# Optimization experiments

Measured on AMD Instinct MI355X. Metric: run time of the kernel, lower is better.

## Reference

```python
import jax, jax.numpy as jnp
import numpy as np

N_NODES = 100000
N_EDGES = 1600000
IN_F = 128
HID_F = 128
OUT_F = 128

def _glorot(key, shape):
    lim = np.sqrt(6.0 / (shape[0] + shape[1]))
    return jax.random.uniform(key, shape, jnp.float32, -lim, lim)

def setup_inputs() -> dict:
    key = jax.random.key(0)
    ks = jax.random.split(key, 9)
    x = jax.random.normal(ks[0], (N_NODES, IN_F), jnp.float32)
    src = jax.random.randint(ks[1], (N_EDGES,), 0, N_NODES, jnp.int32)
    dst = jax.random.randint(ks[2], (N_EDGES,), 0, N_NODES, jnp.int32)
    return {
        'x': x, 'src': src, 'dst': dst,
        'W_self1': _glorot(ks[3], (IN_F, HID_F)),
        'W_neigh1': _glorot(ks[4], (IN_F, HID_F)),
        'b1': jnp.zeros((HID_F,), jnp.float32),
        'W_self2': _glorot(ks[5], (HID_F, OUT_F)),
        'W_neigh2': _glorot(ks[6], (HID_F, OUT_F)),
        'b2': jnp.zeros((OUT_F,), jnp.float32),
    }

def _sage_mean(h, src, dst, W_self, W_neigh, b, n_nodes):
    # mean-aggregate src features onto dst (DGL SAGEConv 'mean')
    msg_sum = jax.ops.segment_sum(h[src], dst, num_segments=n_nodes)  # [N, d]
    deg = jax.ops.segment_sum(jnp.ones_like(dst, jnp.float32), dst, num_segments=n_nodes)
    h_neigh = msg_sum / jnp.maximum(deg, 1.0)[:, None]
    return h @ W_self + h_neigh @ W_neigh + b

def reference(x, src, dst, W_self1, W_neigh1, b1, W_self2, W_neigh2, b2):
    n = x.shape[0]
    h = _sage_mean(x, src, dst, W_self1, W_neigh1, b1, n)
    h = _sage_mean(h, src, dst, W_self2, W_neigh2, b2, n)
    # edge-wise dot product score between endpoint features (u_dot_v)
    s = jnp.sum(h[src] * h[dst], axis=-1)  # [E]
    smin, smax = jnp.min(s), jnp.max(s)
    return (s - smin) / (smax - smin)
```

## Files before the change

### kernel.cpp

```cpp
#include <hip/hip_runtime.h>
#include <hip/hip_bf16.h>

#define F 128

typedef unsigned int uint;
typedef unsigned short ushort;
typedef __attribute__((ext_vector_type(8))) short short8;
typedef __attribute__((ext_vector_type(4))) float f32x4;

__device__ inline ushort f2bf(float f) {
    uint u = __float_as_uint(f);
    u += 0x7FFF + ((u >> 16) & 1);
    return (ushort)(u >> 16);
}
__device__ inline float2 bf2f(uint u) {
    return make_float2(__uint_as_float(u << 16), __uint_as_float(u & 0xFFFF0000u));
}

__global__ __launch_bounds__(256) void rank_kernel(const int* __restrict__ dst,
                                                   int* __restrict__ cnt,
                                                   ushort* __restrict__ rel, int E) {
    int e = blockIdx.x * 256 + threadIdx.x;
    if (e < E) rel[e] = (ushort)atomicAdd(&cnt[dst[e]], 1);
}

__global__ __launch_bounds__(256) void scan_block(const int* __restrict__ cnt,
                                                  int* __restrict__ off,
                                                  int* __restrict__ bsum, int N) {
    __shared__ int t[256];
    int i = blockIdx.x * 256 + threadIdx.x;
    int v = (i < N) ? cnt[i] : 0;
    t[threadIdx.x] = v;
    __syncthreads();
    for (int o = 1; o < 256; o <<= 1) {
        int x = (threadIdx.x >= o) ? t[threadIdx.x - o] : 0;
        __syncthreads();
        t[threadIdx.x] += x;
        __syncthreads();
    }
    if (i < N) off[i] = t[threadIdx.x] - v;
    if (threadIdx.x == 255) bsum[blockIdx.x] = t[255];
}

__global__ __launch_bounds__(512) void scan_sums(int* __restrict__ bsum, int nb) {
    __shared__ int t[512];
    int v = (threadIdx.x < nb) ? bsum[threadIdx.x] : 0;
    t[threadIdx.x] = v;
    __syncthreads();
    for (int o = 1; o < 512; o <<= 1) {
        int x = (threadIdx.x >= o) ? t[threadIdx.x - o] : 0;
        __syncthreads();
        t[threadIdx.x] += x;
        __syncthreads();
    }
    if (threadIdx.x < nb) bsum[threadIdx.x] = t[threadIdx.x] - v;
}

__global__ __launch_bounds__(256) void scan_add_rdeg(int* __restrict__ off,
                                                     const int* __restrict__ bsum,
                                                     const int* __restrict__ cnt,
                                                     float* __restrict__ rdeg, int N) {
    int i = blockIdx.x * 256 + threadIdx.x;
    if (i >= N) return;
    off[i] += bsum[blockIdx.x];
    rdeg[i] = 1.0f / fmaxf((float)cnt[i], 1.0f);
}

__global__ __launch_bounds__(256) void fill_kernel(const int* __restrict__ src,
                                                   const int* __restrict__ dst,
                                                   const int* __restrict__ off,
                                                   const ushort* __restrict__ rel,
                                                   int* __restrict__ srcS, int E) {
    int e = blockIdx.x * 256 + threadIdx.x;
    if (e >= E) return;
    srcS[off[dst[e]] + (int)rel[e]] = src[e];
}

__global__ __launch_bounds__(256) void prep_kernel(const float* __restrict__ x,
                                                   const float* __restrict__ W0,
                                                   const float* __restrict__ W1,
                                                   const float* __restrict__ W2,
                                                   const float* __restrict__ W3,
                                                   uint* __restrict__ xb,
                                                   ushort* __restrict__ Wt, int NF4) {
    int i = blockIdx.x * 256 + threadIdx.x;
    if (i < NF4) {
        float4 v = ((const float4*)x)[i];
        uint ua = (uint)f2bf(v.x) | ((uint)f2bf(v.y) << 16);
        uint ub = (uint)f2bf(v.z) | ((uint)f2bf(v.w) << 16);
        ((uint2*)xb)[i] = make_uint2(ua, ub);
    } else {
        int idx = i - NF4;
        if (idx >= 4 * 16384) return;
        int j    = idx & 7;
        int lane = (idx >> 3) & 63;
        int t    = (idx >> 9) & 7;
        int kk   = (idx >> 12) & 3;
        int mat  = idx >> 14;
        int n = 16 * t + (lane & 15);
        int k = 32 * kk + 8 * (lane >> 4) + j;
        const float* W = (mat == 0) ? W0 : (mat == 1) ? W1 : (mat == 2) ? W2 : W3;
        Wt[idx] = f2bf(W[k * 128 + n]);
    }
}

__global__ __launch_bounds__(256) void agg_gather(const uint* __restrict__ hb,
                                                  const int* __restrict__ off,
                                                  const int* __restrict__ srcS,
                                                  const float* __restrict__ rdeg,
                                                  uint* __restrict__ msgb, int N, int E) {
    int node = blockIdx.x * 4 + (threadIdx.x >> 6);
    int lane = threadIdx.x & 63;
    if (node >= N) return;
    int p = off[node];
    int pe = (node == N - 1) ? E : off[node + 1];
    float2 acc = make_float2(0.f, 0.f);
    if (p < pe) {
        int deg = pe - p;
        int last = pe - 1;
        for (; p < pe; p += 8) {
            int i0 = min(p + 0, last), i1 = min(p + 1, last);
            int i2 = min(p + 2, last), i3 = min(p + 3, last);
            int i4 = min(p + 4, last), i5 = min(p + 5, last);
            int i6 = min(p + 6, last), i7 = min(p + 7, last);
            int s0 = srcS[i0], s1 = srcS[i1], s2 = srcS[i2], s3 = srcS[i3];
            int s4 = srcS[i4], s5 = srcS[i5], s6 = srcS[i6], s7 = srcS[i7];
            float2 f0 = bf2f(hb[(size_t)s0 * 64 + lane]);
            float2 f1 = bf2f(hb[(size_t)s1 * 64 + lane]);
            float2 f2 = bf2f(hb[(size_t)s2 * 64 + lane]);
            float2 f3 = bf2f(hb[(size_t)s3 * 64 + lane]);
            float2 f4 = bf2f(hb[(size_t)s4 * 64 + lane]);
            float2 f5 = bf2f(hb[(size_t)s5 * 64 + lane]);
            float2 f6 = bf2f(hb[(size_t)s6 * 64 + lane]);
            float2 f7 = bf2f(hb[(size_t)s7 * 64 + lane]);
            acc.x += ((f0.x + f1.x) + (f2.x + f3.x)) + ((f4.x + f5.x) + (f6.x + f7.x));
            acc.y += ((f0.y + f1.y) + (f2.y + f3.y)) + ((f4.y + f5.y) + (f6.y + f7.y));
        }
        int d = (8 - (deg & 7)) & 7;
        if (d) {
            float2 fl = bf2f(hb[(size_t)srcS[last] * 64 + lane]);
            float fd = (float)d;
            acc.x -= fd * fl.x;
            acc.y -= fd * fl.y;
        }
    }
    float rd = rdeg[node];
    msgb[(size_t)node * 64 + lane] = (uint)f2bf(acc.x * rd) | ((uint)f2bf(acc.y * rd) << 16);
}

__global__ __launch_bounds__(256) void sage_mfma(const uint* __restrict__ hb,
                                                 const uint* __restrict__ mb,
                                                 const uint* __restrict__ Wt,
                                                 const float* __restrict__ bias,
                                                 ushort* __restrict__ outb, int N) {
    int wave = threadIdx.x >> 6, lane = threadIdx.x & 63;
    int m = lane & 15, q = lane >> 4;
    int r0 = blockIdx.x * 64 + wave * 16;
    int arow = r0 + m;
    if (arow >= N) arow = N - 1;

    f32x4 acc[8];
#pragma unroll
    for (int t = 0; t < 8; t++) acc[t] = (f32x4){0.f, 0.f, 0.f, 0.f};

    const uint* hrow = hb + (size_t)arow * 64;
    const uint* mrow = mb + (size_t)arow * 64;
#pragma unroll
    for (int sel = 0; sel < 2; sel++) {
        const uint* arowp = sel ? mrow : hrow;
        const uint* wsel = Wt + sel * 8192;
#pragma unroll
        for (int kk = 0; kk < 4; kk++) {
            int ko = kk * 16 + q * 4;
            short8 a = *(const short8*)(arowp + ko);
#pragma unroll
            for (int t = 0; t < 8; t++) {
                short8 b = *(const short8*)(wsel + (size_t)((kk * 8 + t) * 64 + lane) * 4);
                acc[t] = __builtin_amdgcn_mfma_f32_16x16x32_bf16(a, b, acc[t], 0, 0, 0);
            }
        }
    }

#pragma unroll
    for (int t = 0; t < 8; t++) {
        float bs = bias[16 * t + m];
#pragma unroll
        for (int r = 0; r < 4; r++) {
            int orow = r0 + q * 4 + r;
            if (orow < N) outb[(size_t)orow * 128 + 16 * t + m] = f2bf(acc[t][r] + bs);
        }
    }
}

__global__ __launch_bounds__(256) void edge_score_mfma(const uint* __restrict__ hb,
                                                       const int* __restrict__ off,
                                                       const int* __restrict__ srcS,
                                                       float* __restrict__ sc,
                                                       float2* __restrict__ pmm, int N, int E) {
    int node = blockIdx.x * 4 + (threadIdx.x >> 6);
    int lane = threadIdx.x & 63;
    int m = lane & 15, q = lane >> 4;
    float lmin = INFINITY, lmax = -INFINITY;

    if (node < N) {
        int p = off[node];
        int pe = (node == N - 1) ? E : off[node + 1];
        if (p < pe) {
            const uint* nrow = hb + (size_t)node * 64;
            short8 bfr[4];
#pragma unroll
            for (int kk = 0; kk < 4; kk++)
                bfr[kk] = *(const short8*)(nrow + kk * 16 + q * 4);

            for (; p < pe; p += 16) {
                int idx = p + m;
                if (idx >= pe) idx = pe - 1;
                const uint* arow = hb + (size_t)srcS[idx] * 64;
                f32x4 acc = (f32x4){0.f, 0.f, 0.f, 0.f};
#pragma unroll
                for (int kk = 0; kk < 4; kk++) {
                    short8 a = *(const short8*)(arow + kk * 16 + q * 4);
                    acc = __builtin_amdgcn_mfma_f32_16x16x32_bf16(a, bfr[kk], acc, 0, 0, 0);
                }
                if (m == 0) {
                    if (p + 16 <= pe) {
                        *(float4*)(sc + p + q * 4) = make_float4(acc[0], acc[1], acc[2], acc[3]);
                        float mn = fminf(fminf(acc[0], acc[1]), fminf(acc[2], acc[3]));
                        float mx = fmaxf(fmaxf(acc[0], acc[1]), fmaxf(acc[2], acc[3]));
                        lmin = fminf(lmin, mn);
                        lmax = fmaxf(lmax, mx);
                    } else {
#pragma unroll
                        for (int r = 0; r < 4; r++) {
                            int e = p + q * 4 + r;
                            if (e < pe) {
                                sc[e] = acc[r];
                                lmin = fminf(lmin, acc[r]);
                                lmax = fmaxf(lmax, acc[r]);
                            }
                        }
                    }
                }
            }
        }
    }

#pragma unroll
    for (int o = 1; o <= 32; o <<= 1) {
        lmin = fminf(lmin, __shfl_xor(lmin, o));
        lmax = fmaxf(lmax, __shfl_xor(lmax, o));
    }
    __shared__ float smin[4], smax[4];
    int wv = threadIdx.x >> 6;
    if (lane == 0) { smin[wv] = lmin; smax[wv] = lmax; }
    __syncthreads();
    if (threadIdx.x == 0) {
        float mA = fminf(fminf(smin[0], smin[1]), fminf(smin[2], smin[3]));
        float MA = fmaxf(fmaxf(smax[0], smax[1]), fmaxf(smax[2], smax[3]));
        pmm[blockIdx.x] = make_float2(mA, MA);
    }
}

__global__ __launch_bounds__(1024) void minmax_final(const float2* __restrict__ pmm,
                                                     float* __restrict__ mmf, int nb) {
    float vmin = INFINITY, vmax = -INFINITY;
    for (int i = threadIdx.x; i < nb; i += 1024) {
        float2 v = pmm[i];
        vmin = fminf(vmin, v.x);
        vmax = fmaxf(vmax, v.y);
    }
#pragma unroll
    for (int o = 1; o <= 32; o <<= 1) {
        vmin = fminf(vmin, __shfl_xor(vmin, o));
        vmax = fmaxf(vmax, __shfl_xor(vmax, o));
    }
    __shared__ float smin[16], smax[16];
    int lane = threadIdx.x & 63, wv = threadIdx.x >> 6;
    if (lane == 0) { smin[wv] = vmin; smax[wv] = vmax; }
    __syncthreads();
    if (threadIdx.x == 0) {
        float m = smin[0], M = smax[0];
        for (int w = 1; w < 16; w++) { m = fminf(m, smin[w]); M = fmaxf(M, smax[w]); }
        mmf[0] = m;
        mmf[1] = M;
    }
}

__global__ __launch_bounds__(256) void norm_kernel(const float* __restrict__ sc,
                                                   const int* __restrict__ dst,
                                                   const ushort* __restrict__ rel,
                                                   const int* __restrict__ off,
                                                   float* __restrict__ out,
                                                   const float* __restrict__ mmf, int E) {
    float mn = mmf[0];
    float mx = mmf[1];
    float inv = 1.0f / (mx - mn);
    int i = blockIdx.x * 256 + threadIdx.x;
    if (i < E) {
        int p = off[dst[i]] + (int)rel[i];
        out[i] = (sc[p] - mn) * inv;
    }
}

extern "C" void kernel_launch(void* const* d_in, const int* in_sizes, int n_in,
                              void* d_out, int out_size, void* d_ws, size_t ws_size,
                              hipStream_t stream) {
    const float* x   = (const float*)d_in[0];
    const int*   src = (const int*)d_in[1];
    const int*   dst = (const int*)d_in[2];
    const float* Ws1 = (const float*)d_in[3];
    const float* Wn1 = (const float*)d_in[4];
    const float* b1  = (const float*)d_in[5];
    const float* Ws2 = (const float*)d_in[6];
    const float* Wn2 = (const float*)d_in[7];
    const float* b2  = (const float*)d_in[8];

    int N = in_sizes[0] / F;
    int E = in_sizes[1];
    float* out = (float*)d_out;

    int nbN = (N + 255) / 256;
    int nbE = (E + 255) / 256;
    int nbEdgeBlocks = (N + 3) / 4;
    int NF4 = N * F / 4;

    int* off  = (int*)d_ws;
    int* cnt  = off + N;
    int* srcS = cnt + N;
    ushort* rel = (ushort*)(srcS + E);
    float* sc = (float*)((int*)rel + E / 2);
    int* bsum = (int*)(sc + E);
    float* rdeg = (float*)(bsum + 1024);
    float* mmf = (float*)(rdeg + N);
    float2* pmm = (float2*)(mmf + 4);
    uint* Wtb = (uint*)(pmm + 25600);
    size_t elemOff = 3 * (size_t)N + 2 * (size_t)E + (size_t)E / 2 + 1024 + 4 + 51200 + 32768;
    elemOff = (elemOff + 3) & ~(size_t)3;
    uint* xb   = (uint*)d_ws + elemOff;
    uint* msgb = xb + (size_t)N * 64;
    uint* h1b  = msgb + (size_t)N * 64;
    uint* h2b  = h1b + (size_t)N * 64;

    hipMemsetAsync(cnt, 0, (size_t)N * sizeof(int), stream);

    rank_kernel<<<nbE, 256, 0, stream>>>(dst, cnt, rel, E);
    scan_block<<<nbN, 256, 0, stream>>>(cnt, off, bsum, N);
    scan_sums<<<1, 512, 0, stream>>>(bsum, nbN);
    scan_add_rdeg<<<nbN, 256, 0, stream>>>(off, bsum, cnt, rdeg, N);
    fill_kernel<<<nbE, 256, 0, stream>>>(src, dst, off, rel, srcS, E);

    prep_kernel<<<(NF4 + 4 * 16384 + 255) / 256, 256, 0, stream>>>(
        x, Ws1, Wn1, Ws2, Wn2, xb, (ushort*)Wtb, NF4);

    agg_gather<<<(N + 3) / 4, 256, 0, stream>>>(xb, off, srcS, rdeg, msgb, N, E);
    sage_mfma<<<(N + 63) / 64, 256, 0, stream>>>(xb, msgb, Wtb, b1, (ushort*)h1b, N);

    agg_gather<<<(N + 3) / 4, 256, 0, stream>>>(h1b, off, srcS, rdeg, msgb, N, E);
    sage_mfma<<<(N + 63) / 64, 256, 0, stream>>>(h1b, msgb, Wtb + 16384, b2, (ushort*)h2b, N);

    edge_score_mfma<<<nbEdgeBlocks, 256, 0, stream>>>(h2b, off, srcS, sc, pmm, N, E);
    minmax_final<<<1, 1024, 0, stream>>>(pmm, mmf, nbEdgeBlocks);
    norm_kernel<<<(E + 255) / 256, 256, 0, stream>>>(sc, dst, rel, off, out, mmf, E);
}
```

Measured before the change: 549.0 us.

## Split gather and edge-score kernels into feature halves mapped to XCD groups

The aggregation kernel now processes each node twice, once per 64-feature half. The block index is remapped so that each half is handled by one group of four XCDs, meaning each XCD's L2 only has to cache half of every feature row. The two halves of a wave gather different edges and combine them with a cross-lane shuffle. Edge scoring is split the same way into two launches over feature halves, with the second launch accumulating into the first launch's scores and computing the min/max. This targets L2 hit rate on random gathers, at the cost of doubled index loads, an extra score read/write pass and an extra kernel launch.

```diff
diff --git a/kernel.cpp b/kernel.cpp
--- a/kernel.cpp
+++ b/kernel.cpp
@@ -104,48 +104,59 @@
     }
 }
 
-__global__ __launch_bounds__(256) void agg_gather(const uint* __restrict__ hb,
-                                                  const int* __restrict__ off,
-                                                  const int* __restrict__ srcS,
-                                                  const float* __restrict__ rdeg,
-                                                  uint* __restrict__ msgb, int N, int E) {
-    int node = blockIdx.x * 4 + (threadIdx.x >> 6);
+__global__ __launch_bounds__(256) void agg_gather_h(const uint* __restrict__ hb,
+                                                    const int* __restrict__ off,
+                                                    const int* __restrict__ srcS,
+                                                    const float* __restrict__ rdeg,
+                                                    uint* __restrict__ msgb, int N, int E) {
+    int g = blockIdx.x;
+    int xcd = g & 7;
+    int half = xcd >> 2;
+    int nb = (g >> 3) * 4 + (xcd & 3);
+    int node = nb * 4 + (threadIdx.x >> 6);
     int lane = threadIdx.x & 63;
+    int l32 = lane & 31;
+    int eh = lane >> 5;
     if (node >= N) return;
+    int hofs = half * 32 + l32;
     int p = off[node];
     int pe = (node == N - 1) ? E : off[node + 1];
     float2 acc = make_float2(0.f, 0.f);
+    int d = 0, last = 0;
     if (p < pe) {
         int deg = pe - p;
-        int last = pe - 1;
+        last = pe - 1;
         for (; p < pe; p += 8) {
-            int i0 = min(p + 0, last), i1 = min(p + 1, last);
-            int i2 = min(p + 2, last), i3 = min(p + 3, last);
-            int i4 = min(p + 4, last), i5 = min(p + 5, last);
-            int i6 = min(p + 6, last), i7 = min(p + 7, last);
-            int s0 = srcS[i0], s1 = srcS[i1], s2 = srcS[i2], s3 = srcS[i3];
-            int s4 = srcS[i4], s5 = srcS[i5], s6 = srcS[i6], s7 = srcS[i7];
-            float2 f0 = bf2f(hb[(size_t)s0 * 64 + lane]);
-            float2 f1 = bf2f(hb[(size_t)s1 * 64 + lane]);
-            float2 f2 = bf2f(hb[(size_t)s2 * 64 + lane]);
-            float2 f3 = bf2f(hb[(size_t)s3 * 64 + lane]);
-            float2 f4 = bf2f(hb[(size_t)s4 * 64 + lane]);
-            float2 f5 = bf2f(hb[(size_t)s5 * 64 + lane]);
-            float2 f6 = bf2f(hb[(size_t)s6 * 64 + lane]);
-            float2 f7 = bf2f(hb[(size_t)s7 * 64 + lane]);
-            acc.x += ((f0.x + f1.x) + (f2.x + f3.x)) + ((f4.x + f5.x) + (f6.x + f7.x));
-            acc.y += ((f0.y + f1.y) + (f2.y + f3.y)) + ((f4.y + f5.y) + (f6.y + f7.y));
-        }
-        int d = (8 - (deg & 7)) & 7;
+            int s0 = srcS[min(p + 0, last)], s1 = srcS[min(p + 1, last)];
+            int s2 = srcS[min(p + 2, last)], s3 = srcS[min(p + 3, last)];
+            int s4 = srcS[min(p + 4, last)], s5 = srcS[min(p + 5, last)];
+            int s6 = srcS[min(p + 6, last)], s7 = srcS[min(p + 7, last)];
+            int a0 = eh ? s1 : s0;
+            int a1 = eh ? s3 : s2;
+            int a2 = eh ? s5 : s4;
+            int a3 = eh ? s7 : s6;
+            float2 f0 = bf2f(hb[(size_t)a0 * 64 + hofs]);
+            float2 f1 = bf2f(hb[(size_t)a1 * 64 + hofs]);
+            float2 f2 = bf2f(hb[(size_t)a2 * 64 + hofs]);
+            float2 f3 = bf2f(hb[(size_t)a3 * 64 + hofs]);
+            acc.x += (f0.x + f1.x) + (f2.x + f3.x);
+            acc.y += (f0.y + f1.y) + (f2.y + f3.y);
+        }
+        d = (8 - (deg & 7)) & 7;
+    }
+    acc.x += __shfl_xor(acc.x, 32);
+    acc.y += __shfl_xor(acc.y, 32);
+    if (eh == 0) {
         if (d) {
-            float2 fl = bf2f(hb[(size_t)srcS[last] * 64 + lane]);
+            float2 fl = bf2f(hb[(size_t)srcS[last] * 64 + hofs]);
             float fd = (float)d;
             acc.x -= fd * fl.x;
             acc.y -= fd * fl.y;
         }
-    }
-    float rd = rdeg[node];
-    msgb[(size_t)node * 64 + lane] = (uint)f2bf(acc.x * rd) | ((uint)f2bf(acc.y * rd) << 16);
+        float rd = rdeg[node];
+        msgb[(size_t)node * 64 + hofs] =
+            (uint)f2bf(acc.x * rd) | ((uint)f2bf(acc.y * rd) << 16);
+    }
 }
 
 __global__ __launch_bounds__(256) void sage_mfma(const uint* __restrict__ hb,
@@ -192,11 +203,12 @@
     }
 }
 
-__global__ __launch_bounds__(256) void edge_score_mfma(const uint* __restrict__ hb,
-                                                       const int* __restrict__ off,
-                                                       const int* __restrict__ srcS,
-                                                       float* __restrict__ sc,
-                                                       float2* __restrict__ pmm, int N, int E) {
+template <int PH>
+__global__ __launch_bounds__(256) void edge_score_h(const uint* __restrict__ hb,
+                                                    const int* __restrict__ off,
+                                                    const int* __restrict__ srcS,
+                                                    float* __restrict__ sc,
+                                                    float2* __restrict__ pmm, int N, int E) {
     int node = blockIdx.x * 4 + (threadIdx.x >> 6);
     int lane = threadIdx.x & 63;
     int m = lane & 15, q = lane >> 4;
@@ -207,10 +219,10 @@
         int pe = (node == N - 1) ? E : off[node + 1];
         if (p < pe) {
             const uint* nrow = hb + (size_t)node * 64;
-            short8 bfr[4];
-#pragma unroll
-            for (int kk = 0; kk < 4; kk++)
-                bfr[kk] = *(const short8*)(nrow + kk * 16 + q * 4);
+            short8 bfr[2];
+#pragma unroll
+            for (int kk = 0; kk < 2; kk++)
+                bfr[kk] = *(const short8*)(nrow + (PH * 2 + kk) * 16 + q * 4);
 
             for (; p < pe; p += 16) {
                 int idx = p + m;
@@ -218,25 +230,37 @@
                 const uint* arow = hb + (size_t)srcS[idx] * 64;
                 f32x4 acc = (f32x4){0.f, 0.f, 0.f, 0.f};
 #pragma unroll
-                for (int kk = 0; kk < 4; kk++) {
-                    short8 a = *(const short8*)(arow + kk * 16 + q * 4);
+                for (int kk = 0; kk < 2; kk++) {
+                    short8 a = *(const short8*)(arow + (PH * 2 + kk) * 16 + q * 4);
                     acc = __builtin_amdgcn_mfma_f32_16x16x32_bf16(a, bfr[kk], acc, 0, 0, 0);
                 }
                 if (m == 0) {
                     if (p + 16 <= pe) {
-                        *(float4*)(sc + p + q * 4) = make_float4(acc[0], acc[1], acc[2], acc[3]);
-                        float mn = fminf(fminf(acc[0], acc[1]), fminf(acc[2], acc[3]));
-                        float mx = fmaxf(fmaxf(acc[0], acc[1]), fmaxf(acc[2], acc[3]));
-                        lmin = fminf(lmin, mn);
-                        lmax = fmaxf(lmax, mx);
+                        if (PH == 0) {
+                            *(float4*)(sc + p + q * 4) =
+                                make_float4(acc[0], acc[1], acc[2], acc[3]);
+                        } else {
+                            float4 o = *(const float4*)(sc + p + q * 4);
+                            o.x += acc[0]; o.y += acc[1]; o.z += acc[2]; o.w += acc[3];
+                            *(float4*)(sc + p + q * 4) = o;
+                            float mn = fminf(fminf(o.x, o.y), fminf(o.z, o.w));
+                            float mx = fmaxf(fmaxf(o.x, o.y), fmaxf(o.z, o.w));
+                            lmin = fminf(lmin, mn);
+                            lmax = fmaxf(lmax, mx);
+                        }
                     } else {
 #pragma unroll
                         for (int r = 0; r < 4; r++) {
                             int e = p + q * 4 + r;
                             if (e < pe) {
-                                sc[e] = acc[r];
-                                lmin = fminf(lmin, acc[r]);
-                                lmax = fmaxf(lmax, acc[r]);
+                                if (PH == 0) {
+                                    sc[e] = acc[r];
+                                } else {
+                                    float o = sc[e] + acc[r];
+                                    sc[e] = o;
+                                    lmin = fminf(lmin, o);
+                                    lmax = fmaxf(lmax, o);
+                                }
                             }
                         }
                     }
@@ -245,19 +269,21 @@
         }
     }
 
-#pragma unroll
-    for (int o = 1; o <= 32; o <<= 1) {
-        lmin = fminf(lmin, __shfl_xor(lmin, o));
-        lmax = fmaxf(lmax, __shfl_xor(lmax, o));
-    }
-    __shared__ float smin[4], smax[4];
-    int wv = threadIdx.x >> 6;
-    if (lane == 0) { smin[wv] = lmin; smax[wv] = lmax; }
-    __syncthreads();
-    if (threadIdx.x == 0) {
-        float mA = fminf(fminf(smin[0], smin[1]), fminf(smin[2], smin[3]));
-        float MA = fmaxf(fmaxf(smax[0], smax[1]), fmaxf(smax[2], smax[3]));
-        pmm[blockIdx.x] = make_float2(mA, MA);
+    if (PH == 1) {
+#pragma unroll
+        for (int o = 1; o <= 32; o <<= 1) {
+            lmin = fminf(lmin, __shfl_xor(lmin, o));
+            lmax = fmaxf(lmax, __shfl_xor(lmax, o));
+        }
+        __shared__ float smin[4], smax[4];
+        int wv = threadIdx.x >> 6;
+        if (lane == 0) { smin[wv] = lmin; smax[wv] = lmax; }
+        __syncthreads();
+        if (threadIdx.x == 0) {
+            float mA = fminf(fminf(smin[0], smin[1]), fminf(smin[2], smin[3]));
+            float MA = fmaxf(fmaxf(smax[0], smax[1]), fmaxf(smax[2], smax[3]));
+            pmm[blockIdx.x] = make_float2(mA, MA);
+        }
     }
 }
 
@@ -352,13 +378,16 @@
     prep_kernel<<<(NF4 + 4 * 16384 + 255) / 256, 256, 0, stream>>>(
         x, Ws1, Wn1, Ws2, Wn2, xb, (ushort*)Wtb, NF4);
 
-    agg_gather<<<(N + 3) / 4, 256, 0, stream>>>(xb, off, srcS, rdeg, msgb, N, E);
+    int nbAggH = 2 * ((N + 3) / 4);
+
+    agg_gather_h<<<nbAggH, 256, 0, stream>>>(xb, off, srcS, rdeg, msgb, N, E);
     sage_mfma<<<(N + 63) / 64, 256, 0, stream>>>(xb, msgb, Wtb, b1, (ushort*)h1b, N);
 
-    agg_gather<<<(N + 3) / 4, 256, 0, stream>>>(h1b, off, srcS, rdeg, msgb, N, E);
+    agg_gather_h<<<nbAggH, 256, 0, stream>>>(h1b, off, srcS, rdeg, msgb, N, E);
     sage_mfma<<<(N + 63) / 64, 256, 0, stream>>>(h1b, msgb, Wtb + 16384, b2, (ushort*)h2b, N);
 
-    edge_score_mfma<<<nbEdgeBlocks, 256, 0, stream>>>(h2b, off, srcS, sc, pmm, N, E);
+    edge_score_h<0><<<nbEdgeBlocks, 256, 0, stream>>>(h2b, off, srcS, sc, pmm, N, E);
+    edge_score_h<1><<<nbEdgeBlocks, 256, 0, stream>>>(h2b, off, srcS, sc, pmm, N, E);
     minmax_final<<<1, 1024, 0, stream>>>(pmm, mmf, nbEdgeBlocks);
     norm_kernel<<<(E + 255) / 256, 256, 0, stream>>>(sc, dst, rel, off, out, mmf, E);
 }
```

After: 668.9 us. 21.8% more time.

## Fuse rank with prep, replace minmax kernel with atomics, add nontemporal hints

Applied to the files above, without the earlier changes.

Merges the edge-rank atomic kernel and the bf16 conversion prep kernel into one launch by splitting the grid on block index. The separate min/max reduction kernel is removed: each edge-score block now does atomicMin/atomicMax on order-preserving uint encodings of its float extremes, with the accumulators reset inside fill_kernel. Nontemporal loads and stores are added for the x read, the msgb write and the msgb read. The aim is fewer launches and less cache pollution, at the cost of global atomic contention on two words.

```diff
diff --git a/kernel.cpp b/kernel.cpp
--- a/kernel.cpp
+++ b/kernel.cpp
@@ -7,6 +7,7 @@
 typedef unsigned short ushort;
 typedef __attribute__((ext_vector_type(8))) short short8;
 typedef __attribute__((ext_vector_type(4))) float f32x4;
+typedef __attribute__((ext_vector_type(4))) uint uint4v;
 
 __device__ inline ushort f2bf(float f) {
     uint u = __float_as_uint(f);
@@ -16,12 +17,50 @@
 __device__ inline float2 bf2f(uint u) {
     return make_float2(__uint_as_float(u << 16), __uint_as_float(u & 0xFFFF0000u));
 }
-
-__global__ __launch_bounds__(256) void rank_kernel(const int* __restrict__ dst,
-                                                   int* __restrict__ cnt,
-                                                   ushort* __restrict__ rel, int E) {
-    int e = blockIdx.x * 256 + threadIdx.x;
-    if (e < E) rel[e] = (ushort)atomicAdd(&cnt[dst[e]], 1);
+__device__ inline uint fenc(float f) {
+    uint u = __float_as_uint(f);
+    return (u & 0x80000000u) ? ~u : (u | 0x80000000u);
+}
+__device__ inline float fdec(uint e) {
+    uint u = (e & 0x80000000u) ? (e ^ 0x80000000u) : ~e;
+    return __uint_as_float(u);
+}
+
+__global__ __launch_bounds__(256) void rank_prep(const int* __restrict__ dst,
+                                                 int* __restrict__ cnt,
+                                                 ushort* __restrict__ rel, int E, int nbE,
+                                                 const float* __restrict__ x,
+                                                 const float* __restrict__ W0,
+                                                 const float* __restrict__ W1,
+                                                 const float* __restrict__ W2,
+                                                 const float* __restrict__ W3,
+                                                 uint* __restrict__ xb,
+                                                 ushort* __restrict__ Wt, int NF4) {
+    int b = blockIdx.x;
+    if (b < nbE) {
+        int e = b * 256 + threadIdx.x;
+        if (e < E) rel[e] = (ushort)atomicAdd(&cnt[dst[e]], 1);
+        return;
+    }
+    int i = (b - nbE) * 256 + threadIdx.x;
+    if (i < NF4) {
+        uint4v u = __builtin_nontemporal_load(((const uint4v*)x) + i);
+        uint ua = (uint)f2bf(__uint_as_float(u.x)) | ((uint)f2bf(__uint_as_float(u.y)) << 16);
+        uint ub = (uint)f2bf(__uint_as_float(u.z)) | ((uint)f2bf(__uint_as_float(u.w)) << 16);
+        ((uint2*)xb)[i] = make_uint2(ua, ub);
+    } else {
+        int idx = i - NF4;
+        if (idx >= 4 * 16384) return;
+        int j    = idx & 7;
+        int lane = (idx >> 3) & 63;
+        int t    = (idx >> 9) & 7;
+        int kk   = (idx >> 12) & 3;
+        int mat  = idx >> 14;
+        int n = 16 * t + (lane & 15);
+        int k = 32 * kk + 8 * (lane >> 4) + j;
+        const float* W = (mat == 0) ? W0 : (mat == 1) ? W1 : (mat == 2) ? W2 : W3;
+        Wt[idx] = f2bf(W[k * 128 + n]);
+    }
 }
 
 __global__ __launch_bounds__(256) void scan_block(const int* __restrict__ cnt,
@@ -70,38 +109,15 @@
                                                    const int* __restrict__ dst,
                                                    const int* __restrict__ off,
                                                    const ushort* __restrict__ rel,
-                                                   int* __restrict__ srcS, int E) {
+                                                   int* __restrict__ srcS,
+                                                   uint* __restrict__ mmfe, int E) {
+    if (blockIdx.x == 0 && threadIdx.x == 0) {
+        mmfe[0] = 0xFFFFFFFFu;
+        mmfe[1] = 0u;
+    }
     int e = blockIdx.x * 256 + threadIdx.x;
     if (e >= E) return;
     srcS[off[dst[e]] + (int)rel[e]] = src[e];
-}
-
-__global__ __launch_bounds__(256) void prep_kernel(const float* __restrict__ x,
-                                                   const float* __restrict__ W0,
-                                                   const float* __restrict__ W1,
-                                                   const float* __restrict__ W2,
-                                                   const float* __restrict__ W3,
-                                                   uint* __restrict__ xb,
-                                                   ushort* __restrict__ Wt, int NF4) {
-    int i = blockIdx.x * 256 + threadIdx.x;
-    if (i < NF4) {
-        float4 v = ((const float4*)x)[i];
-        uint ua = (uint)f2bf(v.x) | ((uint)f2bf(v.y) << 16);
-        uint ub = (uint)f2bf(v.z) | ((uint)f2bf(v.w) << 16);
-        ((uint2*)xb)[i] = make_uint2(ua, ub);
-    } else {
-        int idx = i - NF4;
-        if (idx >= 4 * 16384) return;
-        int j    = idx & 7;
-        int lane = (idx >> 3) & 63;
-        int t    = (idx >> 9) & 7;
-        int kk   = (idx >> 12) & 3;
-        int mat  = idx >> 14;
-        int n = 16 * t + (lane & 15);
-        int k = 32 * kk + 8 * (lane >> 4) + j;
-        const float* W = (mat == 0) ? W0 : (mat == 1) ? W1 : (mat == 2) ? W2 : W3;
-        Wt[idx] = f2bf(W[k * 128 + n]);
-    }
 }
 
 __global__ __launch_bounds__(256) void agg_gather(const uint* __restrict__ hb,
@@ -145,7 +161,8 @@
         }
     }
     float rd = rdeg[node];
-    msgb[(size_t)node * 64 + lane] = (uint)f2bf(acc.x * rd) | ((uint)f2bf(acc.y * rd) << 16);
+    uint w = (uint)f2bf(acc.x * rd) | ((uint)f2bf(acc.y * rd) << 16);
+    __builtin_nontemporal_store(w, msgb + (size_t)node * 64 + lane);
 }
 
 __global__ __launch_bounds__(256) void sage_mfma(const uint* __restrict__ hb,
@@ -167,12 +184,12 @@
     const uint* mrow = mb + (size_t)arow * 64;
 #pragma unroll
     for (int sel = 0; sel < 2; sel++) {
-        const uint* arowp = sel ? mrow : hrow;
         const uint* wsel = Wt + sel * 8192;
 #pragma unroll
         for (int kk = 0; kk < 4; kk++) {
             int ko = kk * 16 + q * 4;
-            short8 a = *(const short8*)(arowp + ko);
+            short8 a = sel ? __builtin_nontemporal_load((const short8*)(mrow + ko))
+                           : *(const short8*)(hrow + ko);
 #pragma unroll
             for (int t = 0; t < 8; t++) {
                 short8 b = *(const short8*)(wsel + (size_t)((kk * 8 + t) * 64 + lane) * 4);
@@ -196,7 +213,7 @@
                                                        const int* __restrict__ off,
                                                        const int* __restrict__ srcS,
                                                        float* __restrict__ sc,
-                                                       float2* __restrict__ pmm, int N, int E) {
+                                                       uint* __restrict__ mmfe, int N, int E) {
     int node = blockIdx.x * 4 + (threadIdx.x >> 6);
     int lane = threadIdx.x & 63;
     int m = lane & 15, q = lane >> 4;
@@ -257,32 +274,8 @@
     if (threadIdx.x == 0) {
         float mA = fminf(fminf(smin[0], smin[1]), fminf(smin[2], smin[3]));
         float MA = fmaxf(fmaxf(smax[0], smax[1]), fmaxf(smax[2], smax[3]));
-        pmm[blockIdx.x] = make_float2(mA, MA);
-    }
-}
-
-__global__ __launch_bounds__(1024) void minmax_final(const float2* __restrict__ pmm,
-                                                     float* __restrict__ mmf, int nb) {
-    float vmin = INFINITY, vmax = -INFINITY;
-    for (int i = threadIdx.x; i < nb; i += 1024) {
-        float2 v = pmm[i];
-        vmin = fminf(vmin, v.x);
-        vmax = fmaxf(vmax, v.y);
-    }
-#pragma unroll
-    for (int o = 1; o <= 32; o <<= 1) {
-        vmin = fminf(vmin, __shfl_xor(vmin, o));
-        vmax = fmaxf(vmax, __shfl_xor(vmax, o));
-    }
-    __shared__ float smin[16], smax[16];
-    int lane = threadIdx.x & 63, wv = threadIdx.x >> 6;
-    if (lane == 0) { smin[wv] = vmin; smax[wv] = vmax; }
-    __syncthreads();
-    if (threadIdx.x == 0) {
-        float m = smin[0], M = smax[0];
-        for (int w = 1; w < 16; w++) { m = fminf(m, smin[w]); M = fmaxf(M, smax[w]); }
-        mmf[0] = m;
-        mmf[1] = M;
+        atomicMin(&mmfe[0], fenc(mA));
+        atomicMax(&mmfe[1], fenc(MA));
     }
 }
 
@@ -291,9 +284,9 @@
                                                    const ushort* __restrict__ rel,
                                                    const int* __restrict__ off,
                                                    float* __restrict__ out,
-                                                   const float* __restrict__ mmf, int E) {
-    float mn = mmf[0];
-    float mx = mmf[1];
+                                                   const uint* __restrict__ mmfe, int E) {
+    float mn = fdec(mmfe[0]);
+    float mx = fdec(mmfe[1]);
     float inv = 1.0f / (mx - mn);
     int i = blockIdx.x * 256 + threadIdx.x;
     if (i < E) {
@@ -331,8 +324,8 @@
     float* sc = (float*)((int*)rel + E / 2);
     int* bsum = (int*)(sc + E);
     float* rdeg = (float*)(bsum + 1024);
-    float* mmf = (float*)(rdeg + N);
-    float2* pmm = (float2*)(mmf + 4);
+    uint* mmfe = (uint*)(rdeg + N);
+    float2* pmm = (float2*)(mmfe + 4);
     uint* Wtb = (uint*)(pmm + 25600);
     size_t elemOff = 3 * (size_t)N + 2 * (size_t)E + (size_t)E / 2 + 1024 + 4 + 51200 + 32768;
     elemOff = (elemOff + 3) & ~(size_t)3;
@@ -341,16 +334,15 @@
     uint* h1b  = msgb + (size_t)N * 64;
     uint* h2b  = h1b + (size_t)N * 64;
 
-    hipMemsetAsync(cnt, 0, (size_t)N * sizeof(int), stream);
-
-    rank_kernel<<<nbE, 256, 0, stream>>>(dst, cnt, rel, E);
+    (void)hipMemsetAsync(cnt, 0, (size_t)N * sizeof(int), stream);
+
+    int nbPrep = (NF4 + 4 * 16384 + 255) / 256;
+    rank_prep<<<nbE + nbPrep, 256, 0, stream>>>(dst, cnt, rel, E, nbE,
+                                                x, Ws1, Wn1, Ws2, Wn2, xb, (ushort*)Wtb, NF4);
     scan_block<<<nbN, 256, 0, stream>>>(cnt, off, bsum, N);
     scan_sums<<<1, 512, 0, stream>>>(bsum, nbN);
     scan_add_rdeg<<<nbN, 256, 0, stream>>>(off, bsum, cnt, rdeg, N);
-    fill_kernel<<<nbE, 256, 0, stream>>>(src, dst, off, rel, srcS, E);
-
-    prep_kernel<<<(NF4 + 4 * 16384 + 255) / 256, 256, 0, stream>>>(
-        x, Ws1, Wn1, Ws2, Wn2, xb, (ushort*)Wtb, NF4);
+    fill_kernel<<<nbE, 256, 0, stream>>>(src, dst, off, rel, srcS, mmfe, E);
 
     agg_gather<<<(N + 3) / 4, 256, 0, stream>>>(xb, off, srcS, rdeg, msgb, N, E);
     sage_mfma<<<(N + 63) / 64, 256, 0, stream>>>(xb, msgb, Wtb, b1, (ushort*)h1b, N);
@@ -358,7 +350,6 @@
     agg_gather<<<(N + 3) / 4, 256, 0, stream>>>(h1b, off, srcS, rdeg, msgb, N, E);
     sage_mfma<<<(N + 63) / 64, 256, 0, stream>>>(h1b, msgb, Wtb + 16384, b2, (ushort*)h2b, N);
 
-    edge_score_mfma<<<nbEdgeBlocks, 256, 0, stream>>>(h2b, off, srcS, sc, pmm, N, E);
-    minmax_final<<<1, 1024, 0, stream>>>(pmm, mmf, nbEdgeBlocks);
-    norm_kernel<<<(E + 255) / 256, 256, 0, stream>>>(sc, dst, rel, off, out, mmf, E);
-}
+    edge_score_mfma<<<nbEdgeBlocks, 256, 0, stream>>>(h2b, off, srcS, sc, mmfe, N, E);
+    norm_kernel<<<(E + 255) / 256, 256, 0, stream>>>(sc, dst, rel, off, out, mmfe, E);
+}
```

Measured after the change: 1.041 ms. 1.9x slower.

## Fuse neighbor aggregation into SAGE MFMA kernel and merge rank with prep

Applied to the files above, without the earlier changes.

Neighbor mean aggregation now happens inside the MFMA layer kernel. Each wave aggregates 16 nodes into a swizzled shared-memory tile, which then feeds the neighbor GEMM directly, so the global msg buffer write and re-read disappear. The edge ranking and the x/W bf16 conversion kernels are merged into one launch, and x is read with nontemporal loads. In exchange, grid parallelism for the gather drops from 4 nodes per block to 64 nodes per block handled serially per wave, which may reduce latency hiding.

```diff
diff --git a/kernel.cpp b/kernel.cpp
--- a/kernel.cpp
+++ b/kernel.cpp
@@ -7,6 +7,7 @@
 typedef unsigned short ushort;
 typedef __attribute__((ext_vector_type(8))) short short8;
 typedef __attribute__((ext_vector_type(4))) float f32x4;
+typedef __attribute__((ext_vector_type(4))) uint uint4v;
 
 __device__ inline ushort f2bf(float f) {
     uint u = __float_as_uint(f);
@@ -17,11 +18,41 @@
     return make_float2(__uint_as_float(u << 16), __uint_as_float(u & 0xFFFF0000u));
 }
 
-__global__ __launch_bounds__(256) void rank_kernel(const int* __restrict__ dst,
-                                                   int* __restrict__ cnt,
-                                                   ushort* __restrict__ rel, int E) {
-    int e = blockIdx.x * 256 + threadIdx.x;
-    if (e < E) rel[e] = (ushort)atomicAdd(&cnt[dst[e]], 1);
+__global__ __launch_bounds__(256) void rank_prep(const int* __restrict__ dst,
+                                                 int* __restrict__ cnt,
+                                                 ushort* __restrict__ rel, int E, int nbE,
+                                                 const float* __restrict__ x,
+                                                 const float* __restrict__ W0,
+                                                 const float* __restrict__ W1,
+                                                 const float* __restrict__ W2,
+                                                 const float* __restrict__ W3,
+                                                 uint* __restrict__ xb,
+                                                 ushort* __restrict__ Wt, int NF4) {
+    int b = blockIdx.x;
+    if (b < nbE) {
+        int e = b * 256 + threadIdx.x;
+        if (e < E) rel[e] = (ushort)atomicAdd(&cnt[dst[e]], 1);
+        return;
+    }
+    int i = (b - nbE) * 256 + threadIdx.x;
+    if (i < NF4) {
+        uint4v u = __builtin_nontemporal_load(((const uint4v*)x) + i);
+        uint ua = (uint)f2bf(__uint_as_float(u.x)) | ((uint)f2bf(__uint_as_float(u.y)) << 16);
+        uint ub = (uint)f2bf(__uint_as_float(u.z)) | ((uint)f2bf(__uint_as_float(u.w)) << 16);
+        ((uint2*)xb)[i] = make_uint2(ua, ub);
+    } else {
+        int idx = i - NF4;
+        if (idx >= 4 * 16384) return;
+        int j    = idx & 7;
+        int lane = (idx >> 3) & 63;
+        int t    = (idx >> 9) & 7;
+        int kk   = (idx >> 12) & 3;
+        int mat  = idx >> 14;
+        int n = 16 * t + (lane & 15);
+        int k = 32 * kk + 8 * (lane >> 4) + j;
+        const float* W = (mat == 0) ? W0 : (mat == 1) ? W1 : (mat == 2) ? W2 : W3;
+        Wt[idx] = f2bf(W[k * 128 + n]);
+    }
 }
 
 __global__ __launch_bounds__(256) void scan_block(const int* __restrict__ cnt,
@@ -76,103 +107,77 @@
     srcS[off[dst[e]] + (int)rel[e]] = src[e];
 }
 
-__global__ __launch_bounds__(256) void prep_kernel(const float* __restrict__ x,
-                                                   const float* __restrict__ W0,
-                                                   const float* __restrict__ W1,
-                                                   const float* __restrict__ W2,
-                                                   const float* __restrict__ W3,
-                                                   uint* __restrict__ xb,
-                                                   ushort* __restrict__ Wt, int NF4) {
-    int i = blockIdx.x * 256 + threadIdx.x;
-    if (i < NF4) {
-        float4 v = ((const float4*)x)[i];
-        uint ua = (uint)f2bf(v.x) | ((uint)f2bf(v.y) << 16);
-        uint ub = (uint)f2bf(v.z) | ((uint)f2bf(v.w) << 16);
-        ((uint2*)xb)[i] = make_uint2(ua, ub);
-    } else {
-        int idx = i - NF4;
-        if (idx >= 4 * 16384) return;
-        int j    = idx & 7;
-        int lane = (idx >> 3) & 63;
-        int t    = (idx >> 9) & 7;
-        int kk   = (idx >> 12) & 3;
-        int mat  = idx >> 14;
-        int n = 16 * t + (lane & 15);
-        int k = 32 * kk + 8 * (lane >> 4) + j;
-        const float* W = (mat == 0) ? W0 : (mat == 1) ? W1 : (mat == 2) ? W2 : W3;
-        Wt[idx] = f2bf(W[k * 128 + n]);
-    }
-}
-
-__global__ __launch_bounds__(256) void agg_gather(const uint* __restrict__ hb,
+__global__ __launch_bounds__(256) void sage_fused(const uint* __restrict__ hb,
                                                   const int* __restrict__ off,
                                                   const int* __restrict__ srcS,
                                                   const float* __restrict__ rdeg,
-                                                  uint* __restrict__ msgb, int N, int E) {
-    int node = blockIdx.x * 4 + (threadIdx.x >> 6);
-    int lane = threadIdx.x & 63;
-    if (node >= N) return;
-    int p = off[node];
-    int pe = (node == N - 1) ? E : off[node + 1];
-    float2 acc = make_float2(0.f, 0.f);
-    if (p < pe) {
-        int deg = pe - p;
-        int last = pe - 1;
-        for (; p < pe; p += 8) {
-            int i0 = min(p + 0, last), i1 = min(p + 1, last);
-            int i2 = min(p + 2, last), i3 = min(p + 3, last);
-            int i4 = min(p + 4, last), i5 = min(p + 5, last);
-            int i6 = min(p + 6, last), i7 = min(p + 7, last);
-            int s0 = srcS[i0], s1 = srcS[i1], s2 = srcS[i2], s3 = srcS[i3];
-            int s4 = srcS[i4], s5 = srcS[i5], s6 = srcS[i6], s7 = srcS[i7];
-            float2 f0 = bf2f(hb[(size_t)s0 * 64 + lane]);
-            float2 f1 = bf2f(hb[(size_t)s1 * 64 + lane]);
-            float2 f2 = bf2f(hb[(size_t)s2 * 64 + lane]);
-            float2 f3 = bf2f(hb[(size_t)s3 * 64 + lane]);
-            float2 f4 = bf2f(hb[(size_t)s4 * 64 + lane]);
-            float2 f5 = bf2f(hb[(size_t)s5 * 64 + lane]);
-            float2 f6 = bf2f(hb[(size_t)s6 * 64 + lane]);
-            float2 f7 = bf2f(hb[(size_t)s7 * 64 + lane]);
-            acc.x += ((f0.x + f1.x) + (f2.x + f3.x)) + ((f4.x + f5.x) + (f6.x + f7.x));
-            acc.y += ((f0.y + f1.y) + (f2.y + f3.y)) + ((f4.y + f5.y) + (f6.y + f7.y));
+                                                  const uint* __restrict__ Wt,
+                                                  const float* __restrict__ bias,
+                                                  ushort* __restrict__ outb, int N, int E) {
+    __shared__ uint lmsg[64][64];
+    int wave = threadIdx.x >> 6, lane = threadIdx.x & 63;
+
+#pragma unroll 1
+    for (int i = 0; i < 16; ++i) {
+        int lr = wave * 16 + i;
+        int node = blockIdx.x * 64 + lr;
+        if (node > N - 1) node = N - 1;
+        int p = off[node];
+        int pe = (node == N - 1) ? E : off[node + 1];
+        float2 acc = make_float2(0.f, 0.f);
+        if (p < pe) {
+            int deg = pe - p;
+            int last = pe - 1;
+            for (; p < pe; p += 8) {
+                int i0 = min(p + 0, last), i1 = min(p + 1, last);
+                int i2 = min(p + 2, last), i3 = min(p + 3, last);
+                int i4 = min(p + 4, last), i5 = min(p + 5, last);
+                int i6 = min(p + 6, last), i7 = min(p + 7, last);
+                int s0 = srcS[i0], s1 = srcS[i1], s2 = srcS[i2], s3 = srcS[i3];
+                int s4 = srcS[i4], s5 = srcS[i5], s6 = srcS[i6], s7 = srcS[i7];
+                float2 f0 = bf2f(hb[(size_t)s0 * 64 + lane]);
+                float2 f1 = bf2f(hb[(size_t)s1 * 64 + lane]);
+                float2 f2 = bf2f(hb[(size_t)s2 * 64 + lane]);
+                float2 f3 = bf2f(hb[(size_t)s3 * 64 + lane]);
+                float2 f4 = bf2f(hb[(size_t)s4 * 64 + lane]);
+                float2 f5 = bf2f(hb[(size_t)s5 * 64 + lane]);
+                float2 f6 = bf2f(hb[(size_t)s6 * 64 + lane]);
+                float2 f7 = bf2f(hb[(size_t)s7 * 64 + lane]);
+                acc.x += ((f0.x + f1.x) + (f2.x + f3.x)) + ((f4.x + f5.x) + (f6.x + f7.x));
+                acc.y += ((f0.y + f1.y) + (f2.y + f3.y)) + ((f4.y + f5.y) + (f6.y + f7.y));
+            }
+            int d = (8 - (deg & 7)) & 7;
+            if (d) {
+                float2 fl = bf2f(hb[(size_t)srcS[last] * 64 + lane]);
+                float fd = (float)d;
+                acc.x -= fd * fl.x;
+                acc.y -= fd * fl.y;
+            }
         }
-        int d = (8 - (deg & 7)) & 7;
-        if (d) {
-            float2 fl = bf2f(hb[(size_t)srcS[last] * 64 + lane]);
-            float fd = (float)d;
-            acc.x -= fd * fl.x;
-            acc.y -= fd * fl.y;
-        }
-    }
-    float rd = rdeg[node];
-    msgb[(size_t)node * 64 + lane] = (uint)f2bf(acc.x * rd) | ((uint)f2bf(acc.y * rd) << 16);
-}
-
-__global__ __launch_bounds__(256) void sage_mfma(const uint* __restrict__ hb,
-                                                 const uint* __restrict__ mb,
-                                                 const uint* __restrict__ Wt,
-                                                 const float* __restrict__ bias,
-                                                 ushort* __restrict__ outb, int N) {
-    int wave = threadIdx.x >> 6, lane = threadIdx.x & 63;
+        float rd = rdeg[node];
+        lmsg[lr][lane ^ ((lr & 15) << 2)] =
+            (uint)f2bf(acc.x * rd) | ((uint)f2bf(acc.y * rd) << 16);
+    }
+
     int m = lane & 15, q = lane >> 4;
     int r0 = blockIdx.x * 64 + wave * 16;
     int arow = r0 + m;
     if (arow >= N) arow = N - 1;
+    const uint* hrow = hb + (size_t)arow * 64;
+    int lrm = wave * 16 + m;
 
     f32x4 acc[8];
 #pragma unroll
     for (int t = 0; t < 8; t++) acc[t] = (f32x4){0.f, 0.f, 0.f, 0.f};
 
-    const uint* hrow = hb + (size_t)arow * 64;
-    const uint* mrow = mb + (size_t)arow * 64;
 #pragma unroll
     for (int sel = 0; sel < 2; sel++) {
-        const uint* arowp = sel ? mrow : hrow;
         const uint* wsel = Wt + sel * 8192;
 #pragma unroll
         for (int kk = 0; kk < 4; kk++) {
             int ko = kk * 16 + q * 4;
-            short8 a = *(const short8*)(arowp + ko);
+            short8 a = sel ? *(const short8*)&lmsg[lrm][ko ^ (m << 2)]
+                           : *(const short8*)(hrow + ko);
 #pragma unroll
             for (int t = 0; t < 8; t++) {
                 short8 b = *(const short8*)(wsel + (size_t)((kk * 8 + t) * 64 + lane) * 4);
@@ -337,26 +342,23 @@
     size_t elemOff = 3 * (size_t)N + 2 * (size_t)E + (size_t)E / 2 + 1024 + 4 + 51200 + 32768;
     elemOff = (elemOff + 3) & ~(size_t)3;
     uint* xb   = (uint*)d_ws + elemOff;
-    uint* msgb = xb + (size_t)N * 64;
-    uint* h1b  = msgb + (size_t)N * 64;
+    uint* h1b  = xb + (size_t)N * 64;
     uint* h2b  = h1b + (size_t)N * 64;
 
-    hipMemsetAsync(cnt, 0, (size_t)N * sizeof(int), stream);
-
-    rank_kernel<<<nbE, 256, 0, stream>>>(dst, cnt, rel, E);
+    (void)hipMemsetAsync(cnt, 0, (size_t)N * sizeof(int), stream);
+
+    int nbPrep = (NF4 + 4 * 16384 + 255) / 256;
+    rank_prep<<<nbE + nbPrep, 256, 0, stream>>>(dst, cnt, rel, E, nbE,
+                                                x, Ws1, Wn1, Ws2, Wn2, xb, (ushort*)Wtb, NF4);
     scan_block<<<nbN, 256, 0, stream>>>(cnt, off, bsum, N);
     scan_sums<<<1, 512, 0, stream>>>(bsum, nbN);
     scan_add_rdeg<<<nbN, 256, 0, stream>>>(off, bsum, cnt, rdeg, N);
     fill_kernel<<<nbE, 256, 0, stream>>>(src, dst, off, rel, srcS, E);
 
-    prep_kernel<<<(NF4 + 4 * 16384 + 255) / 256, 256, 0, stream>>>(
-        x, Ws1, Wn1, Ws2, Wn2, xb, (ushort*)Wtb, NF4);
-
-    agg_gather<<<(N + 3) / 4, 256, 0, stream>>>(xb, off, srcS, rdeg, msgb, N, E);
-    sage_mfma<<<(N + 63) / 64, 256, 0, stream>>>(xb, msgb, Wtb, b1, (ushort*)h1b, N);
-
-    agg_gather<<<(N + 3) / 4, 256, 0, stream>>>(h1b, off, srcS, rdeg, msgb, N, E);
-    sage_mfma<<<(N + 63) / 64, 256, 0, stream>>>(h1b, msgb, Wtb + 16384, b2, (ushort*)h2b, N);
+    int nbSage = (N + 63) / 64;
+    sage_fused<<<nbSage, 256, 0, stream>>>(xb, off, srcS, rdeg, Wtb, b1, (ushort*)h1b, N, E);
+    sage_fused<<<nbSage, 256, 0, stream>>>(h1b, off, srcS, rdeg, Wtb + 16384, b2,
+                                           (ushort*)h2b, N, E);
 
     edge_score_mfma<<<nbEdgeBlocks, 256, 0, stream>>>(h2b, off, srcS, sc, pmm, N, E);
     minmax_final<<<1, 1024, 0, stream>>>(pmm, mmf, nbEdgeBlocks);
```

Result: slower. 579.3 us (+5.5%).
